# Kernel tuning notes

Measured on AMD Instinct MI355X. Metric: run time of the kernel, lower is better.

Reference implementation:

```python
import jax, jax.numpy as jnp
import numpy as np

N_NODES = 262144          # 8192 graphs * 32 nodes
N_EDGES = 2097152         # avg degree 8
C_IN = 64
C_HID = 64
C_OUT_GCN = 64            # 'output' layer -> channel_out = 64
NODES_PER_BATCH = 32
FC_IN = NODES_PER_BATCH * C_OUT_GCN   # 2048
FC_HID = 256
OUT_DIM = 32
NEG_SLOPE = 0.2


def setup_inputs() -> dict:
    key = jax.random.key(0)
    ks = jax.random.split(key, 16)
    def glorot(k, shape):
        fan_in, fan_out = shape[0], shape[-1]
        lim = jnp.sqrt(6.0 / (fan_in + fan_out))
        return jax.random.uniform(k, shape, jnp.float32, -lim, lim)
    inp = {
        "x": jax.random.normal(ks[0], (N_NODES, C_IN), jnp.float32),
        "edge_index": jax.random.randint(ks[1], (2, N_EDGES), 0, N_NODES, jnp.int64),
        # GATConv layer 1
        "W1": glorot(ks[2], (C_IN, C_HID)),
        "att_src1": glorot(ks[3], (C_HID,)),
        "att_dst1": glorot(ks[4], (C_HID,)),
        "b1": jnp.zeros((C_HID,), jnp.float32),
        # GATConv layer 2
        "W2": glorot(ks[5], (C_HID, C_OUT_GCN)),
        "att_src2": glorot(ks[6], (C_OUT_GCN,)),
        "att_dst2": glorot(ks[7], (C_OUT_GCN,)),
        "b2": jnp.zeros((C_OUT_GCN,), jnp.float32),
        # FC head
        "Wf1": glorot(ks[8], (FC_IN, FC_HID)),
        "bf1": jnp.zeros((FC_HID,), jnp.float32),
        "Wf2": glorot(ks[9], (FC_HID, OUT_DIM)),
        "bf2": jnp.zeros((OUT_DIM,), jnp.float32),
    }
    return inp


def gat_conv(x, src, dst, W, att_src, att_dst, bias):
    """PyG GATConv, heads=1, add_self_loops=False. Message flows src -> dst."""
    h = x @ W                                  # [N, C]
    a_s = h @ att_src                          # [N]
    a_d = h @ att_dst                          # [N]
    e = a_s[src] + a_d[dst]                    # [E]
    e = jnp.where(e > 0, e, NEG_SLOPE * e)     # leaky_relu
    n = x.shape[0]
    # segment softmax over edges grouped by target node
    m = jax.ops.segment_max(e, dst, num_segments=n)
    e = jnp.exp(e - m[dst])
    s = jax.ops.segment_sum(e, dst, num_segments=n)
    alpha = e / s[dst]                         # s[dst] > 0 for every existing edge
    msg = alpha[:, None] * h[src]              # [E, C]
    out = jax.ops.segment_sum(msg, dst, num_segments=n)
    return out + bias


def reference(x, edge_index, W1, att_src1, att_dst1, b1,
              W2, att_src2, att_dst2, b2, Wf1, bf1, Wf2, bf2):
    src, dst = edge_index[0], edge_index[1]
    h = gat_conv(x, src, dst, W1, att_src1, att_dst1, b1)
    h = gat_conv(h, src, dst, W2, att_src2, att_dst2, b2)
    num_batch = h.shape[0] // NODES_PER_BATCH
    g = h.reshape(num_batch, -1)               # [B, 32*64]
    f = jax.nn.relu(g @ Wf1 + bf1)
    return f @ Wf2 + bf2                       # [B, 32]
```

## Files before the change

### kernel.cpp

```cpp
#include <hip/hip_runtime.h>
#include <stdint.h>

#define N_NODES_C 262144
#define N_EDGES_C 2097152
#define NB_C      8192
#define NEG_SLOPE_C 0.2f

#define NBKT 1024
#define NPB  256
#define CHUNK 8192
#define NBINBLK 256

typedef __attribute__((ext_vector_type(4))) float f32x4;
typedef __attribute__((ext_vector_type(8))) short short8;
typedef __attribute__((ext_vector_type(4))) unsigned short us4;
typedef unsigned int u32;

static __device__ __forceinline__ unsigned short f2bf(float f) {
    unsigned int u = __builtin_bit_cast(unsigned int, f);
    unsigned int r = (u + 0x7FFFu + ((u >> 16) & 1u)) >> 16;
    return (unsigned short)r;
}
static __device__ __forceinline__ float bf2f(unsigned short u) {
    unsigned int x = ((unsigned int)u) << 16;
    return __builtin_bit_cast(float, x);
}

__global__ void zero_u32(u32* __restrict__ p, int n) {
    int i = blockIdx.x * blockDim.x + threadIdx.x;
    int stride = gridDim.x * blockDim.x;
    for (int k = i; k < n; k += stride) p[k] = 0u;
}

__global__ void transpose_cast(const float* __restrict__ in,
                               unsigned short* __restrict__ out, int R, int Cc) {
    int i = blockIdx.x * blockDim.x + threadIdx.x;
    if (i < R * Cc) {
        int r = i / Cc, c = i % Cc;
        out[(size_t)c * R + r] = f2bf(in[i]);
    }
}

__global__ __launch_bounds__(256) void bin_count(const int* __restrict__ dst,
                                                 u32* __restrict__ gtotal) {
    __shared__ u32 hist[NBKT];
    for (int i = threadIdx.x; i < NBKT; i += 256) hist[i] = 0u;
    __syncthreads();
    const int e0 = blockIdx.x * CHUNK;
    for (int i = threadIdx.x; i < CHUNK; i += 256)
        atomicAdd(&hist[((u32)dst[e0 + i]) >> 8], 1u);
    __syncthreads();
    for (int i = threadIdx.x; i < NBKT; i += 256)
        if (hist[i]) atomicAdd(&gtotal[i], hist[i]);
}

__global__ __launch_bounds__(256) void bin_scan(const u32* __restrict__ gtotal,
                                                u32* __restrict__ cbase,
                                                u32* __restrict__ gcursor) {
    __shared__ u32 sd[256];
    const int t = threadIdx.x;
    uint4 c = ((const uint4*)gtotal)[t];
    u32 s = c.x + c.y + c.z + c.w;
    sd[t] = s;
    __syncthreads();
    for (int off = 1; off < 256; off <<= 1) {
        u32 v = (t >= off) ? sd[t - off] : 0u;
        __syncthreads();
        sd[t] += v;
        __syncthreads();
    }
    u32 ex = sd[t] - s;
    u32 b0 = ex, b1 = ex + c.x, b2 = b1 + c.y, b3 = b2 + c.z;
    cbase[t * 4 + 0] = b0; gcursor[t * 4 + 0] = b0;
    cbase[t * 4 + 1] = b1; gcursor[t * 4 + 1] = b1;
    cbase[t * 4 + 2] = b2; gcursor[t * 4 + 2] = b2;
    cbase[t * 4 + 3] = b3; gcursor[t * 4 + 3] = b3;
    if (t == 255) cbase[NBKT] = N_EDGES_C;
}

__global__ __launch_bounds__(256) void bin_scatter(const int* __restrict__ src,
                                                   const int* __restrict__ dst,
                                                   u32* __restrict__ gcursor,
                                                   u32* __restrict__ packed) {
    __shared__ u32 hist[NBKT];
    __shared__ u32 gpos[NBKT];
    __shared__ u32 cur[NBKT];
    for (int i = threadIdx.x; i < NBKT; i += 256) { hist[i] = 0u; cur[i] = 0u; }
    __syncthreads();
    const int e0 = blockIdx.x * CHUNK;
    for (int i = threadIdx.x; i < CHUNK; i += 256)
        atomicAdd(&hist[((u32)dst[e0 + i]) >> 8], 1u);
    __syncthreads();
    for (int i = threadIdx.x; i < NBKT; i += 256) {
        u32 c = hist[i];
        gpos[i] = c ? atomicAdd(&gcursor[i], c) : 0u;
    }
    __syncthreads();
    for (int i = threadIdx.x; i < CHUNK; i += 256) {
        u32 d = (u32)dst[e0 + i];
        u32 b = d >> 8;
        u32 r = atomicAdd(&cur[b], 1u);
        packed[gpos[b] + r] = (u32)src[e0 + i] | ((d & 255u) << 18);
    }
}

__global__ __launch_bounds__(256) void csr_convert(const u32* __restrict__ cbase,
                                                   const u32* __restrict__ packed,
                                                   u32* __restrict__ row_start,
                                                   int* __restrict__ sorted_src) {
    __shared__ u32 cnt[NPB];
    __shared__ u32 pos[NPB];
    const int b = blockIdx.x;
    const u32 beg = cbase[b], end = cbase[b + 1];
    const int t = threadIdx.x;
    cnt[t] = 0u;
    __syncthreads();
    for (u32 i = beg + t; i < end; i += 256)
        atomicAdd(&cnt[packed[i] >> 18], 1u);
    __syncthreads();
    pos[t] = cnt[t];
    __syncthreads();
    for (int off = 1; off < 256; off <<= 1) {
        u32 v = (t >= off) ? pos[t - off] : 0u;
        __syncthreads();
        pos[t] += v;
        __syncthreads();
    }
    const u32 ex = pos[t] - cnt[t];
    row_start[b * NPB + t] = beg + ex;
    __syncthreads();
    cnt[t] = ex;
    __syncthreads();
    for (u32 i = beg + t; i < end; i += 256) {
        u32 p = packed[i];
        u32 r = atomicAdd(&cnt[p >> 18], 1u);
        sorted_src[beg + r] = (int)(p & 0x3FFFFu);
    }
    if (b == 0 && t == 0) row_start[N_NODES_C] = N_EDGES_C;
}

template <int LAYER>
__global__ __launch_bounds__(256) void transform_mfma(
    const void* __restrict__ xin_,
    const unsigned short* __restrict__ Wt,
    const float* __restrict__ att_s, const float* __restrict__ att_d,
    const float* __restrict__ bias_in,
    unsigned short* __restrict__ h_bf,
    float* __restrict__ a_s, float* __restrict__ a_d)
{
    const int lane = threadIdx.x & 63;
    const int wid  = threadIdx.x >> 6;
    const int col  = lane & 15;
    const int kl   = lane >> 4;

    short8 bfr[4][2];
    #pragma unroll
    for (int t = 0; t < 4; ++t)
        #pragma unroll
        for (int kh = 0; kh < 2; ++kh)
            bfr[t][kh] = *(const short8*)(Wt + (t * 16 + col) * 64 + kh * 32 + kl * 8);

    float attS[4], attD[4];
    #pragma unroll
    for (int t = 0; t < 4; ++t) {
        attS[t] = att_s[t * 16 + col];
        attD[t] = att_d[t * 16 + col];
    }
    float bofs[2][8];
    if constexpr (LAYER == 2) {
        #pragma unroll
        for (int kh = 0; kh < 2; ++kh)
            #pragma unroll
            for (int j = 0; j < 8; ++j) bofs[kh][j] = bias_in[kh * 32 + kl * 8 + j];
    }

    const int g = blockIdx.x * 4 + wid;
    const int arow = g * 16 + col;
    short8 af[2];
    if constexpr (LAYER == 1) {
        const float* xp = (const float*)xin_ + (size_t)arow * 64;
        #pragma unroll
        for (int kh = 0; kh < 2; ++kh) {
            f32x4 v0 = *(const f32x4*)(xp + kh * 32 + kl * 8);
            f32x4 v1 = *(const f32x4*)(xp + kh * 32 + kl * 8 + 4);
            short8 a;
            #pragma unroll
            for (int j = 0; j < 4; ++j) {
                a[j]     = (short)f2bf(v0[j]);
                a[4 + j] = (short)f2bf(v1[j]);
            }
            af[kh] = a;
        }
    } else {
        const unsigned short* xp = (const unsigned short*)xin_ + (size_t)arow * 64;
        #pragma unroll
        for (int kh = 0; kh < 2; ++kh) {
            short8 raw = *(const short8*)(xp + kh * 32 + kl * 8);
            short8 a;
            #pragma unroll
            for (int j = 0; j < 8; ++j)
                a[j] = (short)f2bf(bf2f((unsigned short)raw[j]) + bofs[kh][j]);
            af[kh] = a;
        }
    }

    f32x4 acc[4];
    #pragma unroll
    for (int t = 0; t < 4; ++t) {
        f32x4 d = {0.f, 0.f, 0.f, 0.f};
        d = __builtin_amdgcn_mfma_f32_16x16x32_bf16(af[0], bfr[t][0], d, 0, 0, 0);
        d = __builtin_amdgcn_mfma_f32_16x16x32_bf16(af[1], bfr[t][1], d, 0, 0, 0);
        acc[t] = d;
    }

    float ps[4] = {0.f, 0.f, 0.f, 0.f}, pd[4] = {0.f, 0.f, 0.f, 0.f};
    #pragma unroll
    for (int t = 0; t < 4; ++t) {
        #pragma unroll
        for (int j = 0; j < 4; ++j) {
            int node = g * 16 + kl * 4 + j;
            h_bf[(size_t)node * 64 + t * 16 + col] = f2bf(acc[t][j]);
            ps[j] += acc[t][j] * attS[t];
            pd[j] += acc[t][j] * attD[t];
        }
    }
    #pragma unroll
    for (int m = 1; m < 16; m <<= 1) {
        #pragma unroll
        for (int j = 0; j < 4; ++j) {
            ps[j] += __shfl_xor(ps[j], m, 64);
            pd[j] += __shfl_xor(pd[j], m, 64);
        }
    }
    if (col == 0) {
        #pragma unroll
        for (int j = 0; j < 4; ++j) {
            int node = g * 16 + kl * 4 + j;
            a_s[node] = ps[j];
            a_d[node] = pd[j];
        }
    }
}

static __device__ __forceinline__ void agg_one_node(
    int node, u32 beg, u32 end, int lane, int sub, int c4,
    const int* __restrict__ sorted_src, const float* __restrict__ a_s,
    const float* __restrict__ a_d, const unsigned short* __restrict__ h_bf,
    const float* __restrict__ bias_out, unsigned short* __restrict__ agg_bf)
{
    f32x4 acc = {0.f, 0.f, 0.f, 0.f};
    if (end > beg) {
        const float ad = a_d[node];
        float l = 0.f;
        for (u32 base = beg; base < end; base += 64) {
            u32 i = base + lane;
            bool valid = i < end;
            int s = valid ? sorted_src[i] : 0;
            float e = valid ? a_s[s] + ad : 0.f;
            e = e > 0.f ? e : NEG_SLOPE_C * e;
            float p = valid ? __expf(e) : 0.f;
            #pragma unroll
            for (int off = 32; off; off >>= 1) p += __shfl_xor(p, off, 64);
            l += p;
        }
        const float inv = 1.f / l;
        for (u32 base = beg; base < end; base += 64) {
            u32 i = base + lane;
            bool valid = i < end;
            int s = valid ? sorted_src[i] : 0;
            float e = valid ? a_s[s] + ad : 0.f;
            e = e > 0.f ? e : NEG_SLOPE_C * e;
            float p = valid ? __expf(e) * inv : 0.f;
            int c2 = (int)min(64u, end - base);
            for (int t = 0; t < c2; t += 4) {
                int j = t + sub;
                float al = __shfl(p, j, 64);
                int   sj = __shfl(s, j, 64);
                if (j >= c2) al = 0.f;
                us4 hv = *(const us4*)(h_bf + (size_t)sj * 64 + c4);
                acc[0] += al * bf2f(hv[0]);
                acc[1] += al * bf2f(hv[1]);
                acc[2] += al * bf2f(hv[2]);
                acc[3] += al * bf2f(hv[3]);
            }
        }
    }
    #pragma unroll
    for (int k = 0; k < 4; ++k) {
        acc[k] += __shfl_xor(acc[k], 16, 64);
        acc[k] += __shfl_xor(acc[k], 32, 64);
    }
    if (sub == 0) {
        us4 o;
        if (bias_out) {
            #pragma unroll
            for (int k = 0; k < 4; ++k) o[k] = f2bf(acc[k] + bias_out[c4 + k]);
        } else {
            #pragma unroll
            for (int k = 0; k < 4; ++k) o[k] = f2bf(acc[k]);
        }
        *(us4*)(agg_bf + (size_t)node * 64 + c4) = o;
    }
}

__global__ __launch_bounds__(256) void gat_aggregate(
    const u32* __restrict__ row_start, const int* __restrict__ sorted_src,
    const float* __restrict__ a_s, const float* __restrict__ a_d,
    const unsigned short* __restrict__ h_bf, const float* __restrict__ bias_out,
    unsigned short* __restrict__ agg_bf)
{
    const int lane = threadIdx.x & 63;
    const int sub  = lane >> 4;
    const int c4   = (lane & 15) * 4;
    const int wid = (blockIdx.x * blockDim.x + threadIdx.x) >> 6;
    const int n0 = wid * 4;

    uint4 r4 = *(const uint4*)(row_start + n0);
    u32 rs[5] = { r4.x, r4.y, r4.z, r4.w, row_start[n0 + 4] };
    const u32 beg = rs[0], end = rs[4];
    const int tot = (int)(end - beg);

    if (tot > 64) {
        #pragma unroll
        for (int k = 0; k < 4; ++k)
            agg_one_node(n0 + k, rs[k], rs[k + 1], lane, sub, c4,
                         sorted_src, a_s, a_d, h_bf, bias_out, agg_bf);
        return;
    }

    const u32 i = beg + (u32)lane;
    const bool valid = i < end;
    int s = valid ? sorted_src[i] : 0;
    const u32 r1 = rs[1] - beg, r2 = rs[2] - beg, r3 = rs[3] - beg;
    const int nid = (int)((u32)lane >= r1) + (int)((u32)lane >= r2) + (int)((u32)lane >= r3);
    float e = valid ? a_s[s] + a_d[n0 + nid] : 0.f;
    e = e > 0.f ? e : NEG_SLOPE_C * e;
    const float p = valid ? __expf(e) : 0.f;

    float l0 = (nid == 0) ? p : 0.f;
    float l1 = (nid == 1) ? p : 0.f;
    float l2 = (nid == 2) ? p : 0.f;
    float l3 = (nid == 3) ? p : 0.f;
    #pragma unroll
    for (int off = 32; off; off >>= 1) {
        l0 += __shfl_xor(l0, off, 64);
        l1 += __shfl_xor(l1, off, 64);
        l2 += __shfl_xor(l2, off, 64);
        l3 += __shfl_xor(l3, off, 64);
    }
    const float i0 = 1.f / l0, i1 = 1.f / l1, i2 = 1.f / l2, i3 = 1.f / l3;
    const float invk = (nid < 2) ? (nid == 0 ? i0 : i1) : (nid == 2 ? i2 : i3);
    const float alpha = valid ? p * invk : 0.f;

    #pragma unroll
    for (int k = 0; k < 4; ++k) {
        const int rb = (int)(rs[k] - beg);
        const int ck = (int)(rs[k + 1] - rs[k]);
        f32x4 acc = {0.f, 0.f, 0.f, 0.f};
        for (int t = 0; t < ck; t += 8) {
            const int j0 = rb + t + sub;
            const int j1 = j0 + 4;
            float al0 = __shfl(alpha, j0, 64);
            int   s0  = __shfl(s, j0, 64);
            float al1 = __shfl(alpha, j1, 64);
            int   s1  = __shfl(s, j1, 64);
            if (t + sub >= ck)     al0 = 0.f;
            if (t + 4 + sub >= ck) al1 = 0.f;
            us4 h0 = *(const us4*)(h_bf + (size_t)s0 * 64 + c4);
            us4 h1 = *(const us4*)(h_bf + (size_t)s1 * 64 + c4);
            acc[0] += al0 * bf2f(h0[0]) + al1 * bf2f(h1[0]);
            acc[1] += al0 * bf2f(h0[1]) + al1 * bf2f(h1[1]);
            acc[2] += al0 * bf2f(h0[2]) + al1 * bf2f(h1[2]);
            acc[3] += al0 * bf2f(h0[3]) + al1 * bf2f(h1[3]);
        }
        #pragma unroll
        for (int q = 0; q < 4; ++q) {
            acc[q] += __shfl_xor(acc[q], 16, 64);
            acc[q] += __shfl_xor(acc[q], 32, 64);
        }
        if (sub == 0) {
            us4 o;
            if (bias_out) {
                #pragma unroll
                for (int q = 0; q < 4; ++q) o[q] = f2bf(acc[q] + bias_out[c4 + q]);
            } else {
                #pragma unroll
                for (int q = 0; q < 4; ++q) o[q] = f2bf(acc[q]);
            }
            *(us4*)(agg_bf + (size_t)(n0 + k) * 64 + c4) = o;
        }
    }
}

__global__ __launch_bounds__(512) void fc1_mfma(
    const unsigned short* __restrict__ agg_bf,
    const unsigned short* __restrict__ Wf1t,
    const float* __restrict__ bf1, float* __restrict__ fbuf)
{
    __shared__ float sh[4][64][33];
    const int lane = threadIdx.x & 63;
    const int w    = threadIdx.x >> 6;
    const int cg   = w & 3;
    const int kh   = w >> 2;
    const int col  = lane & 15;
    const int kl   = lane >> 4;
    const int rbase = blockIdx.x * 32;

    const int kbase = kh * 1024 + kl * 8;
    const unsigned short* a0p = agg_bf + (size_t)(rbase + col) * 2048 + kbase;
    const unsigned short* a1p = a0p + 16 * 2048;
    const unsigned short* bp0 = Wf1t + (size_t)(cg * 64 + col) * 2048 + kbase;
    const unsigned short* bp1 = bp0 + 16 * 2048;
    const unsigned short* bp2 = bp0 + 32 * 2048;
    const unsigned short* bp3 = bp0 + 48 * 2048;

    f32x4 acc[2][4];
    #pragma unroll
    for (int rt = 0; rt < 2; ++rt)
        #pragma unroll
        for (int ct = 0; ct < 4; ++ct) acc[rt][ct] = (f32x4){0.f, 0.f, 0.f, 0.f};

    short8 a0 = *(const short8*)a0p, a1 = *(const short8*)a1p;
    short8 b0 = *(const short8*)bp0, b1 = *(const short8*)bp1;
    short8 b2 = *(const short8*)bp2, b3 = *(const short8*)bp3;

    for (int ks = 0; ks < 32; ++ks) {
        const short8 ca0 = a0, ca1 = a1, cb0 = b0, cb1 = b1, cb2 = b2, cb3 = b3;
        if (ks < 31) {
            const int off = (ks + 1) * 32;
            a0 = *(const short8*)(a0p + off);
            a1 = *(const short8*)(a1p + off);
            b0 = *(const short8*)(bp0 + off);
            b1 = *(const short8*)(bp1 + off);
            b2 = *(const short8*)(bp2 + off);
            b3 = *(const short8*)(bp3 + off);
        }
        acc[0][0] = __builtin_amdgcn_mfma_f32_16x16x32_bf16(ca0, cb0, acc[0][0], 0, 0, 0);
        acc[1][0] = __builtin_amdgcn_mfma_f32_16x16x32_bf16(ca1, cb0, acc[1][0], 0, 0, 0);
        acc[0][1] = __builtin_amdgcn_mfma_f32_16x16x32_bf16(ca0, cb1, acc[0][1], 0, 0, 0);
        acc[1][1] = __builtin_amdgcn_mfma_f32_16x16x32_bf16(ca1, cb1, acc[1][1], 0, 0, 0);
        acc[0][2] = __builtin_amdgcn_mfma_f32_16x16x32_bf16(ca0, cb2, acc[0][2], 0, 0, 0);
        acc[1][2] = __builtin_amdgcn_mfma_f32_16x16x32_bf16(ca1, cb2, acc[1][2], 0, 0, 0);
        acc[0][3] = __builtin_amdgcn_mfma_f32_16x16x32_bf16(ca0, cb3, acc[0][3], 0, 0, 0);
        acc[1][3] = __builtin_amdgcn_mfma_f32_16x16x32_bf16(ca1, cb3, acc[1][3], 0, 0, 0);
    }

    if (kh == 1) {
        #pragma unroll
        for (int rt = 0; rt < 2; ++rt)
            #pragma unroll
            for (int ct = 0; ct < 4; ++ct)
                #pragma unroll
                for (int j = 0; j < 4; ++j)
                    sh[cg][lane][rt * 16 + ct * 4 + j] = acc[rt][ct][j];
    }
    __syncthreads();
    if (kh == 0) {
        #pragma unroll
        for (int rt = 0; rt < 2; ++rt) {
            #pragma unroll
            for (int ct = 0; ct < 4; ++ct) {
                const int ocol = cg * 64 + ct * 16 + col;
                const float bias = bf1[ocol];
                #pragma unroll
                for (int j = 0; j < 4; ++j) {
                    int row = rbase + rt * 16 + kl * 4 + j;
                    float v = acc[rt][ct][j] + sh[cg][lane][rt * 16 + ct * 4 + j] + bias;
                    fbuf[(size_t)row * 256 + ocol] = v > 0.f ? v : 0.f;
                }
            }
        }
    }
}

__global__ __launch_bounds__(256) void fc2_f32(
    const float* __restrict__ fbuf, const float* __restrict__ Wf2,
    const float* __restrict__ bf2v, float* __restrict__ out)
{
    __shared__ float w[256 * 32];
    for (int i = threadIdx.x; i < 256 * 32; i += 256) w[i] = Wf2[i];
    __syncthreads();
    int tid = blockIdx.x * 256 + threadIdx.x;
    int b = tid >> 5, o = tid & 31;
    float acc = bf2v[o];
    const float* fp = fbuf + (size_t)b * 256;
    for (int j = 0; j < 256; j += 4) {
        f32x4 f4 = *(const f32x4*)(fp + j);
        acc += f4[0] * w[(j + 0) * 32 + o];
        acc += f4[1] * w[(j + 1) * 32 + o];
        acc += f4[2] * w[(j + 2) * 32 + o];
        acc += f4[3] * w[(j + 3) * 32 + o];
    }
    out[(size_t)b * 32 + o] = acc;
}

extern "C" void kernel_launch(void* const* d_in, const int* in_sizes, int n_in,
                              void* d_out, int out_size, void* d_ws, size_t ws_size,
                              hipStream_t stream)
{
    const float* x    = (const float*)d_in[0];
    const int*   ei   = (const int*)d_in[1];
    const float* W1   = (const float*)d_in[2];
    const float* as1  = (const float*)d_in[3];
    const float* ad1  = (const float*)d_in[4];
    const float* b1   = (const float*)d_in[5];
    const float* W2   = (const float*)d_in[6];
    const float* as2  = (const float*)d_in[7];
    const float* ad2  = (const float*)d_in[8];
    const float* b2   = (const float*)d_in[9];
    const float* Wf1  = (const float*)d_in[10];
    const float* bf1  = (const float*)d_in[11];
    const float* Wf2  = (const float*)d_in[12];
    const float* bf2v = (const float*)d_in[13];

    const int* src = ei;
    const int* dst = ei + N_EDGES_C;

    char* ws = (char*)d_ws;
    unsigned short* h_bf   = (unsigned short*)ws; ws += (size_t)N_NODES_C * 64 * 2;
    unsigned short* agg_bf = (unsigned short*)ws; ws += (size_t)N_NODES_C * 64 * 2;
    float* a_s          = (float*)ws;          ws += (size_t)N_NODES_C * 4;
    float* a_d          = (float*)ws;          ws += (size_t)N_NODES_C * 4;
    u32* row_start      = (u32*)ws;            ws += (size_t)(N_NODES_C + 4) * 4;
    int* sorted_src     = (int*)ws;            ws += (size_t)N_EDGES_C * 4;
    u32* packed         = (u32*)ws;            ws += (size_t)N_EDGES_C * 4;
    u32* gtotal         = (u32*)ws;            ws += NBKT * 4;
    u32* cbase          = (u32*)ws;            ws += (NBKT + 4) * 4;
    u32* gcursor        = (u32*)ws;            ws += NBKT * 4;
    float* fbuf         = (float*)ws;          ws += (size_t)NB_C * 256 * 4;
    unsigned short* Wt1 = (unsigned short*)ws; ws += 64 * 64 * 2;
    unsigned short* Wt2 = (unsigned short*)ws; ws += 64 * 64 * 2;
    unsigned short* Wf1t = (unsigned short*)ws; ws += (size_t)256 * 2048 * 2;

    transpose_cast<<<16, 256, 0, stream>>>(W1, Wt1, 64, 64);
    transpose_cast<<<16, 256, 0, stream>>>(W2, Wt2, 64, 64);
    transpose_cast<<<2048, 256, 0, stream>>>(Wf1, Wf1t, 2048, 256);

    zero_u32<<<1, 256, 0, stream>>>(gtotal, NBKT);
    bin_count<<<NBINBLK, 256, 0, stream>>>(dst, gtotal);
    bin_scan<<<1, 256, 0, stream>>>(gtotal, cbase, gcursor);
    bin_scatter<<<NBINBLK, 256, 0, stream>>>(src, dst, gcursor, packed);
    csr_convert<<<NBKT, 256, 0, stream>>>(cbase, packed, row_start, sorted_src);

    transform_mfma<1><<<4096, 256, 0, stream>>>(x, Wt1, as1, ad1, nullptr, h_bf, a_s, a_d);
    gat_aggregate<<<16384, 256, 0, stream>>>(row_start, sorted_src, a_s, a_d, h_bf,
                                             nullptr, agg_bf);

    transform_mfma<2><<<4096, 256, 0, stream>>>(agg_bf, Wt2, as2, ad2, b1, h_bf, a_s, a_d);
    gat_aggregate<<<16384, 256, 0, stream>>>(row_start, sorted_src, a_s, a_d, h_bf,
                                             b2, agg_bf);

    fc1_mfma<<<256, 512, 0, stream>>>(agg_bf, Wf1t, bf1, fbuf);
    fc2_f32<<<1024, 256, 0, stream>>>(fbuf, Wf2, bf2v, (float*)d_out);
}
```

Baseline: 332.5 us.

## Assign one 16-lane subgroup per node in GAT aggregation fast path

The small-degree path of the aggregation kernel used to walk the four nodes one after another, with all four 16-lane subgroups splitting each node's edges and then reducing across subgroups with shuffles. Now each subgroup owns one node and loops up to the largest degree among the four, two edges per step. This removes the cross-subgroup shuffle reductions and the serial per-node loop, at the cost of idle lanes when degrees are uneven. The rs array is also unpacked into scalars.

```diff
diff --git a/kernel.cpp b/kernel.cpp
--- a/kernel.cpp
+++ b/kernel.cpp
@@ -316,22 +316,23 @@
     const int n0 = wid * 4;
 
     uint4 r4 = *(const uint4*)(row_start + n0);
-    u32 rs[5] = { r4.x, r4.y, r4.z, r4.w, row_start[n0 + 4] };
-    const u32 beg = rs[0], end = rs[4];
+    const u32 rs0 = r4.x, rs1 = r4.y, rs2 = r4.z, rs3 = r4.w;
+    const u32 rs4 = row_start[n0 + 4];
+    const u32 beg = rs0, end = rs4;
     const int tot = (int)(end - beg);
 
     if (tot > 64) {
-        #pragma unroll
-        for (int k = 0; k < 4; ++k)
-            agg_one_node(n0 + k, rs[k], rs[k + 1], lane, sub, c4,
-                         sorted_src, a_s, a_d, h_bf, bias_out, agg_bf);
+        agg_one_node(n0 + 0, rs0, rs1, lane, sub, c4, sorted_src, a_s, a_d, h_bf, bias_out, agg_bf);
+        agg_one_node(n0 + 1, rs1, rs2, lane, sub, c4, sorted_src, a_s, a_d, h_bf, bias_out, agg_bf);
+        agg_one_node(n0 + 2, rs2, rs3, lane, sub, c4, sorted_src, a_s, a_d, h_bf, bias_out, agg_bf);
+        agg_one_node(n0 + 3, rs3, rs4, lane, sub, c4, sorted_src, a_s, a_d, h_bf, bias_out, agg_bf);
         return;
     }
 
     const u32 i = beg + (u32)lane;
     const bool valid = i < end;
     int s = valid ? sorted_src[i] : 0;
-    const u32 r1 = rs[1] - beg, r2 = rs[2] - beg, r3 = rs[3] - beg;
+    const u32 r1 = rs1 - beg, r2 = rs2 - beg, r3 = rs3 - beg;
     const int nid = (int)((u32)lane >= r1) + (int)((u32)lane >= r2) + (int)((u32)lane >= r3);
     float e = valid ? a_s[s] + a_d[n0 + nid] : 0.f;
     e = e > 0.f ? e : NEG_SLOPE_C * e;
@@ -352,44 +353,40 @@
     const float invk = (nid < 2) ? (nid == 0 ? i0 : i1) : (nid == 2 ? i2 : i3);
     const float alpha = valid ? p * invk : 0.f;
 
-    #pragma unroll
-    for (int k = 0; k < 4; ++k) {
-        const int rb = (int)(rs[k] - beg);
-        const int ck = (int)(rs[k + 1] - rs[k]);
-        f32x4 acc = {0.f, 0.f, 0.f, 0.f};
-        for (int t = 0; t < ck; t += 8) {
-            const int j0 = rb + t + sub;
-            const int j1 = j0 + 4;
-            float al0 = __shfl(alpha, j0, 64);
-            int   s0  = __shfl(s, j0, 64);
-            float al1 = __shfl(alpha, j1, 64);
-            int   s1  = __shfl(s, j1, 64);
-            if (t + sub >= ck)     al0 = 0.f;
-            if (t + 4 + sub >= ck) al1 = 0.f;
-            us4 h0 = *(const us4*)(h_bf + (size_t)s0 * 64 + c4);
-            us4 h1 = *(const us4*)(h_bf + (size_t)s1 * 64 + c4);
-            acc[0] += al0 * bf2f(h0[0]) + al1 * bf2f(h1[0]);
-            acc[1] += al0 * bf2f(h0[1]) + al1 * bf2f(h1[1]);
-            acc[2] += al0 * bf2f(h0[2]) + al1 * bf2f(h1[2]);
-            acc[3] += al0 * bf2f(h0[3]) + al1 * bf2f(h1[3]);
-        }
-        #pragma unroll
-        for (int q = 0; q < 4; ++q) {
-            acc[q] += __shfl_xor(acc[q], 16, 64);
-            acc[q] += __shfl_xor(acc[q], 32, 64);
-        }
-        if (sub == 0) {
-            us4 o;
-            if (bias_out) {
-                #pragma unroll
-                for (int q = 0; q < 4; ++q) o[q] = f2bf(acc[q] + bias_out[c4 + q]);
-            } else {
-                #pragma unroll
-                for (int q = 0; q < 4; ++q) o[q] = f2bf(acc[q]);
-            }
-            *(us4*)(agg_bf + (size_t)(n0 + k) * 64 + c4) = o;
-        }
-    }
+    const u32 rlo = (sub == 0) ? rs0 : (sub == 1) ? rs1 : (sub == 2) ? rs2 : rs3;
+    const u32 rhi = (sub == 0) ? rs1 : (sub == 1) ? rs2 : (sub == 2) ? rs3 : rs4;
+    const int rb = (int)(rlo - beg);
+    const int ck = (int)(rhi - rlo);
+    const int mx = max(max((int)(rs1 - rs0), (int)(rs2 - rs1)),
+                       max((int)(rs3 - rs2), (int)(rs4 - rs3)));
+
+    f32x4 acc = {0.f, 0.f, 0.f, 0.f};
+    for (int t = 0; t < mx; t += 2) {
+        const int j0 = rb + t;
+        const int j1 = j0 + 1;
+        float al0 = __shfl(alpha, j0, 64);
+        int   s0  = __shfl(s, j0, 64);
+        float al1 = __shfl(alpha, j1, 64);
+        int   s1  = __shfl(s, j1, 64);
+        if (t >= ck)     al0 = 0.f;
+        if (t + 1 >= ck) al1 = 0.f;
+        us4 h0 = *(const us4*)(h_bf + (size_t)s0 * 64 + c4);
+        us4 h1 = *(const us4*)(h_bf + (size_t)s1 * 64 + c4);
+        acc[0] += al0 * bf2f(h0[0]) + al1 * bf2f(h1[0]);
+        acc[1] += al0 * bf2f(h0[1]) + al1 * bf2f(h1[1]);
+        acc[2] += al0 * bf2f(h0[2]) + al1 * bf2f(h1[2]);
+        acc[3] += al0 * bf2f(h0[3]) + al1 * bf2f(h1[3]);
+    }
+
+    us4 o;
+    if (bias_out) {
+        #pragma unroll
+        for (int q = 0; q < 4; ++q) o[q] = f2bf(acc[q] + bias_out[c4 + q]);
+    } else {
+        #pragma unroll
+        for (int q = 0; q < 4; ++q) o[q] = f2bf(acc[q]);
+    }
+    *(us4*)(agg_bf + (size_t)(n0 + sub) * 64 + c4) = o;
 }
 
 __global__ __launch_bounds__(512) void fc1_mfma(
```

Result: faster. 307.2 us (-7.6%).
